# Performance work log

Measured on AMD Instinct MI355X. Metric: run time of the kernel, lower is better.

The kernel has to match this reference:

```python
import jax, jax.numpy as jnp
import numpy as np
from jax import lax

B, CIN, COUT, K, SDIM, H = 8, 512, 512, 3, 512, 32
EPS = 1e-8
LRELU_SLOPE = 0.2
ACT_SCALE = float(np.sqrt(2.0))


def setup_inputs() -> dict:
    key = jax.random.key(0)
    k1, k2, k3, k4 = jax.random.split(key, 4)
    return {
        "x": jax.random.normal(k1, (B, CIN, H, H), jnp.float32),
        "style": jax.random.normal(k2, (B, SDIM), jnp.float32),
        "weight": jax.random.normal(k3, (COUT, CIN, K, K), jnp.float32),
        "mod_w": jax.random.normal(k4, (CIN, SDIM), jnp.float32),
        "mod_b": jnp.ones((CIN,), jnp.float32),  # EqualLinear bias_init=1
        "bias": jnp.zeros((COUT,), jnp.float32),  # FusedLeakyReLU bias
    }


def _blur_kernel(c):
    bk = np.array([1.0, 3.0, 3.0, 1.0], np.float32)
    bk = bk[None, :] * bk[:, None]
    bk = bk / bk.sum() * 4.0  # upsample_factor ** 2
    return jnp.tile(jnp.asarray(bk)[None, None], (c, 1, 1, 1))  # (C,1,4,4)


def reference(x, style, weight, mod_w, mod_b, bias):
    b, cin, h, w = x.shape
    cout, k = weight.shape[0], weight.shape[-1]
    conv_scale = 1.0 / np.sqrt(cin * k * k)
    lin_scale = 1.0 / np.sqrt(mod_w.shape[1])

    # style modulation: EqualLinear(style_dim -> in_channel), bias_init=1
    s = style @ (mod_w * lin_scale).T + mod_b  # (B, Cin)

    # per-sample modulated weights (B, Cout, Cin, k, k)
    wmod = conv_scale * weight[None] * s[:, None, :, None, None]
    demod = lax.rsqrt(jnp.sum(wmod * wmod, axis=(2, 3, 4)) + EPS)
    wmod = wmod * demod[:, :, None, None, None]

    # conv_transpose2d(stride=2, pad=0) == conv with lhs_dilation=2, pad=k-1,
    # spatially-flipped kernel (torch transposes (Cout,Cin)->(Cin,Cout)).
    wflip = jnp.flip(wmod, (-2, -1))

    def convt(xi, wi):  # xi: (Cin,H,W), wi: (Cout,Cin,k,k)
        return lax.conv_general_dilated(
            xi[None], wi, (1, 1), [(k - 1, k - 1)] * 2,
            lhs_dilation=(2, 2),
            dimension_numbers=("NCHW", "OIHW", "NCHW"))[0]

    y = jax.vmap(convt)(x, wflip)  # (B, Cout, 2H+1, 2W+1)

    # Blur: upfirdn2d with pad=(1,1), depthwise 4x4 FIR (kernel symmetric)
    bk = _blur_kernel(cout)
    y = lax.conv_general_dilated(
        y, bk, (1, 1), [(1, 1), (1, 1)],
        feature_group_count=cout,
        dimension_numbers=("NCHW", "OIHW", "NCHW"))  # (B, Cout, 2H, 2W)

    # FusedLeakyReLU: leaky_relu(y + bias) * sqrt(2)
    z = y + bias[None, :, None, None]
    return jnp.where(z >= 0, z, LRELU_SLOPE * z) * ACT_SCALE
```

## Files before the change

kernel.cpp:

```cpp
#include <hip/hip_runtime.h>
#include <hip/hip_bf16.h>

#define NB 8
#define CIN 512
#define COUT 512
#define SDIM 512

typedef __attribute__((ext_vector_type(8))) short short8;
typedef __attribute__((ext_vector_type(4))) float f32x4;

static constexpr float CONV_SCALE = 0.014731391274719740f;
static constexpr float LIN_SCALE  = 0.044194173824159216f;

static constexpr size_t OFF_S     = 0;
static constexpr size_t OFF_WSQ   = 16384;
static constexpr size_t OFF_DEMOD = 1064960;
static constexpr size_t OFF_XP    = 1081344;
static constexpr size_t OFF_WP    = 10551296;
static constexpr size_t OFF_Y1    = 15269888;
static constexpr size_t XP_BYTES  = 9469952;

__device__ __forceinline__ int wpoff(int ps) {
  return ps == 0 ? 0 : ps == 1 ? 1048576 : ps == 2 ? 1572864 : 2097152;
}
__device__ __forceinline__ constexpr int y1off(int ps) {
  return ps == 0 ? 0 : ps == 1 ? 4460544 : ps == 2 ? 8785920 : 13111296;
}

__device__ __forceinline__ short f2bf(float f) {
  unsigned u = __builtin_bit_cast(unsigned, f);
  unsigned r = (u + 0x7fffu + ((u >> 16) & 1u)) >> 16;
  return (short)r;
}

__device__ __forceinline__ void load_lds16(const short* g, short* l) {
  __builtin_amdgcn_global_load_lds(
      (const __attribute__((address_space(1))) unsigned int*)g,
      (__attribute__((address_space(3))) unsigned int*)l, 16, 0, 0);
}

__global__ void k_style(const float* __restrict__ style, const float* __restrict__ mod_w,
                        const float* __restrict__ mod_b, float* __restrict__ s_out) {
  int wid = threadIdx.x >> 6, lane = threadIdx.x & 63;
  int ci = blockIdx.x * 4 + wid;
  float acc[NB] = {};
  for (int k = lane; k < SDIM; k += 64) {
    float wm = mod_w[ci * SDIM + k];
#pragma unroll
    for (int b = 0; b < NB; ++b) acc[b] += wm * style[b * SDIM + k];
  }
#pragma unroll
  for (int b = 0; b < NB; ++b) {
    float v = acc[b];
    for (int o = 32; o > 0; o >>= 1) v += __shfl_xor(v, o);
    if (lane == 0) s_out[b * CIN + ci] = v * LIN_SCALE + mod_b[ci];
  }
}

__global__ void k_wprep(const float* __restrict__ w, short* __restrict__ wp,
                        float* __restrict__ wsq) {
  int idx = blockIdx.x * blockDim.x + threadIdx.x;
  int co = idx >> 9, ci = idx & 511;
  float wv[3][3];
  float sq = 0.f;
#pragma unroll
  for (int i = 0; i < 9; ++i) {
    float v = w[idx * 9 + i];
    wv[i / 3][i % 3] = v;
    sq += v * v;
  }
  wsq[idx] = sq * CONV_SCALE * CONV_SCALE;
#pragma unroll
  for (int wy = 0; wy < 3; ++wy)
#pragma unroll
    for (int wx = 0; wx < 3; ++wx) {
      int psy = (wy == 1) ? 1 : 0, psx = (wx == 1) ? 1 : 0;
      int u = psy ? 0 : (wy == 0 ? 1 : 0);
      int v = psx ? 0 : (wx == 0 ? 1 : 0);
      int ps = psy * 2 + psx;
      int tap = psy ? (psx ? 0 : v) : (psx ? u : u * 2 + v);
      int k = tap * 512 + ci;
      int elem = wpoff(ps) + ((k >> 6) * 512 + co) * 64 + (k & 63);
      wp[elem] = f2bf(wv[wy][wx] * CONV_SCALE);
    }
}

__global__ void k_demod(const float* __restrict__ wsq, const float* __restrict__ s,
                        float* __restrict__ demod) {
  int wid = threadIdx.x >> 6, lane = threadIdx.x & 63;
  int co = blockIdx.x * 4 + wid;
  float acc[NB] = {};
  for (int ci = lane; ci < CIN; ci += 64) {
    float wq = wsq[co * CIN + ci];
#pragma unroll
    for (int b = 0; b < NB; ++b) {
      float sv = s[b * CIN + ci];
      acc[b] += wq * sv * sv;
    }
  }
#pragma unroll
  for (int b = 0; b < NB; ++b) {
    float v = acc[b];
    for (int o = 32; o > 0; o >>= 1) v += __shfl_xor(v, o);
    if (lane == 0) demod[b * COUT + co] = rsqrtf(v + 1e-8f);
  }
}

__global__ void k_xprep(const float* __restrict__ x, const float* __restrict__ s,
                        short* __restrict__ xp) {
  __shared__ float t[64][65];
  int sp0 = blockIdx.x * 64, ci0 = blockIdx.y * 64, b = blockIdx.z;
  for (int r = threadIdx.y; r < 64; r += 4)
    t[r][threadIdx.x] = x[(b * CIN + ci0 + r) * 1024 + sp0 + threadIdx.x];
  __syncthreads();
  int ci = ci0 + threadIdx.x;
  float sv = s[b * CIN + ci];
  for (int r = threadIdx.y; r < 64; r += 4) {
    int sp = sp0 + r;
    int yy = sp >> 5, xx = sp & 31;
    xp[((b * 34 + yy + 1) * 34 + (xx + 1)) * 512 + ci] = f2bf(t[threadIdx.x][r] * sv);
  }
}

__global__ __launch_bounds__(256, 2) void k_gemm(const short* __restrict__ xp,
                                                 const short* __restrict__ wp,
                                                 float* __restrict__ y1) {
  int ps = blockIdx.z;
  int psy = ps >> 1, psx = ps & 1;
  int Ny = 33 - psy, Nx = 33 - psx;
  int N = NB * Ny * Nx;
  int n0 = blockIdx.x * 128;
  if (n0 >= N) return;
  int m0 = blockIdx.y * 128;
  int KT = (2 - psy) * (2 - psx) * 8;
  const short* wpb = wp + wpoff(ps);
  float* y1b = y1 + y1off(ps);

  __shared__ short sW[128 * 64];
  __shared__ short sX[128 * 64];

  int tid = threadIdx.x;
  int wid = tid >> 6, lane = tid & 63;

  int bb[4], ay[4], ax[4];
#pragma unroll
  for (int i = 0; i < 4; ++i) {
    int seg = i * 256 + tid;
    int n = n0 + (seg >> 3);
    if (n >= N) n = N - 1;
    int b = n / (Ny * Nx);
    int rem = n - b * (Ny * Nx);
    int a_y = rem / Nx;
    bb[i] = b; ay[i] = a_y; ax[i] = rem - a_y * Nx;
  }
  int kseg8 = (tid & 7) * 8;

  f32x4 acc[4][4] = {};

  for (int kt = 0; kt < KT; ++kt) {
    int tap = kt >> 3, ci0 = (kt & 7) << 6;
    int oy, ox;
    if (ps == 0)      { oy = tap >> 1; ox = tap & 1; }
    else if (ps == 1) { oy = tap;      ox = 1; }
    else if (ps == 2) { oy = 1;        ox = tap; }
    else              { oy = 1;        ox = 1; }
#pragma unroll
    for (int i = 0; i < 4; ++i) {
      int seg = i * 256 + tid;
      const short* g = wpb + (kt * 512 + m0 + (seg >> 3)) * 64 + kseg8;
      load_lds16(g, &sW[(i * 4 + wid) * 512]);
    }
#pragma unroll
    for (int i = 0; i < 4; ++i) {
      const short* g = xp + ((bb[i] * 34 + ay[i] + oy) * 34 + ax[i] + ox) * 512 + ci0 + kseg8;
      load_lds16(g, &sX[(i * 4 + wid) * 512]);
    }
    asm volatile("s_waitcnt vmcnt(0)" ::: "memory");
    __syncthreads();

    int wm = (wid >> 1) * 64, wn = (wid & 1) * 64;
#pragma unroll
    for (int ks = 0; ks < 2; ++ks) {
      short8 af[4], bf[4];
#pragma unroll
      for (int mf = 0; mf < 4; ++mf)
        af[mf] = *(const short8*)&sW[(wm + mf * 16 + (lane & 15)) * 64 + ks * 32 + (lane >> 4) * 8];
#pragma unroll
      for (int nf = 0; nf < 4; ++nf)
        bf[nf] = *(const short8*)&sX[(wn + nf * 16 + (lane & 15)) * 64 + ks * 32 + (lane >> 4) * 8];
#pragma unroll
      for (int mf = 0; mf < 4; ++mf)
#pragma unroll
        for (int nf = 0; nf < 4; ++nf)
          acc[mf][nf] = __builtin_amdgcn_mfma_f32_16x16x32_bf16(af[mf], bf[nf], acc[mf][nf], 0, 0, 0);
    }
    __syncthreads();
  }

  int wm = (wid >> 1) * 64, wn = (wid & 1) * 64;
#pragma unroll
  for (int mf = 0; mf < 4; ++mf) {
    int m = m0 + wm + mf * 16 + (lane >> 4) * 4;
#pragma unroll
    for (int nf = 0; nf < 4; ++nf) {
      int n = n0 + wn + nf * 16 + (lane & 15);
      if (n < N) {
#pragma unroll
        for (int r = 0; r < 4; ++r) y1b[(m + r) * N + n] = acc[mf][nf][r];
      }
    }
  }
}

__global__ __launch_bounds__(256, 4) void k_blur(const float* __restrict__ y1,
                                                 const float* __restrict__ demod,
                                                 const float* __restrict__ bias,
                                                 float* __restrict__ out) {
  __shared__ float sin_[4][35 * 35];
  __shared__ float stmp[2][35][64];
  const int tid = threadIdx.x;
  const int bc = blockIdx.x;
  const int co = bc & 511, b = bc >> 9;

  for (int i = tid; i < 4 * 35 * 35; i += 256) ((float*)sin_)[i] = 0.f;
  __syncthreads();

#pragma unroll
  for (int ps = 0; ps < 4; ++ps) {
    const int Nyv = 33 - (ps >> 1), Nxv = 33 - (ps & 1);
    const float* pl = y1 + y1off(ps) + (co * NB + b) * (Nyv * Nxv);
    for (int t = tid; t < Nyv * Nxv; t += 256) {
      int av = t / Nxv, ah = t - av * Nxv;
      sin_[ps][(av + 1) * 35 + ah + 1] = pl[t];
    }
  }
  __syncthreads();

  const int q = tid & 63;
  const int mx = q >> 1, fx = q & 1;
  int xp0, xi0, xp1, xi1, xp2, xi2, xp3, xi3;
  if (fx) { xp0 = 0; xi0 = mx + 1; xp1 = 1; xi1 = mx + 1; xp2 = 0; xi2 = mx + 2; xp3 = 1; xi3 = mx + 2; }
  else    { xp0 = 1; xi0 = mx;     xp1 = 0; xi1 = mx + 1; xp2 = 1; xi2 = mx + 1; xp3 = 0; xi3 = mx + 2; }

  for (int r = tid >> 6; r < 70; r += 4) {
    int pv = (r >= 35) ? 1 : 0;
    int av = r - pv * 35;
    float v = 0.25f * sin_[pv * 2 + xp0][av * 35 + xi0]
            + 0.75f * sin_[pv * 2 + xp1][av * 35 + xi1]
            + 0.75f * sin_[pv * 2 + xp2][av * 35 + xi2]
            + 0.25f * sin_[pv * 2 + xp3][av * 35 + xi3];
    stmp[pv][av][q] = v;
  }
  __syncthreads();

  const float dm = demod[b * COUT + co], bs = bias[co];
  for (int p = tid >> 6; p < 64; p += 4) {
    int my = p >> 1, fy = p & 1;
    float v;
    if (fy) v = 0.25f * stmp[0][my + 1][q] + 0.75f * stmp[1][my + 1][q]
              + 0.75f * stmp[0][my + 2][q] + 0.25f * stmp[1][my + 2][q];
    else    v = 0.25f * stmp[1][my][q]     + 0.75f * stmp[0][my + 1][q]
              + 0.75f * stmp[1][my + 1][q] + 0.25f * stmp[0][my + 2][q];
    float val = dm * v + bs;
    out[(bc * 64 + p) * 64 + q] = (val >= 0.f ? val : 0.2f * val) * 1.41421356237309515f;
  }
}

extern "C" void kernel_launch(void* const* d_in, const int* in_sizes, int n_in,
                              void* d_out, int out_size, void* d_ws, size_t ws_size,
                              hipStream_t stream) {
  const float* x      = (const float*)d_in[0];
  const float* style  = (const float*)d_in[1];
  const float* weight = (const float*)d_in[2];
  const float* mod_w  = (const float*)d_in[3];
  const float* mod_b  = (const float*)d_in[4];
  const float* bias   = (const float*)d_in[5];
  float* out = (float*)d_out;
  char* ws = (char*)d_ws;

  float* s     = (float*)(ws + OFF_S);
  float* wsq   = (float*)(ws + OFF_WSQ);
  float* demod = (float*)(ws + OFF_DEMOD);
  short* xp    = (short*)(ws + OFF_XP);
  short* wp    = (short*)(ws + OFF_WP);
  float* y1    = (float*)(ws + OFF_Y1);

  hipMemsetAsync(xp, 0, XP_BYTES, stream);
  k_style<<<128, 256, 0, stream>>>(style, mod_w, mod_b, s);
  k_wprep<<<1024, 256, 0, stream>>>(weight, wp, wsq);
  k_demod<<<128, 256, 0, stream>>>(wsq, s, demod);
  k_xprep<<<dim3(16, 8, 8), dim3(64, 4), 0, stream>>>(x, s, xp);
  k_gemm<<<dim3(69, 4, 4), 256, 0, stream>>>(xp, wp, y1);
  k_blur<<<4096, 256, 0, stream>>>(y1, demod, bias, out);
}
```

Measured before the change: 142.6 us.

## Make GEMM persistent with atomic ticket work queue across parity phases

```diff
diff --git a/kernel.cpp b/kernel.cpp
--- a/kernel.cpp
+++ b/kernel.cpp
@@ -19,6 +19,9 @@
 static constexpr size_t OFF_WP    = 10551296;
 static constexpr size_t OFF_Y1    = 15269888;
 static constexpr size_t XP_BYTES  = 9469952;
+static constexpr size_t OFF_TICKET = OFF_WSQ;
+
+static constexpr int NJOBS = 1060;
 
 __device__ __forceinline__ int wpoff(int ps) {
   return ps == 0 ? 0 : ps == 1 ? 1048576 : ps == 2 ? 1572864 : 2097152;
@@ -124,89 +127,102 @@
 
 __global__ __launch_bounds__(256, 2) void k_gemm(const short* __restrict__ xp,
                                                  const short* __restrict__ wp,
-                                                 float* __restrict__ y1) {
-  int ps = blockIdx.z;
-  int psy = ps >> 1, psx = ps & 1;
-  int Ny = 33 - psy, Nx = 33 - psx;
-  int N = NB * Ny * Nx;
-  int n0 = blockIdx.x * 128;
-  if (n0 >= N) return;
-  int m0 = blockIdx.y * 128;
-  int KT = (2 - psy) * (2 - psx) * 8;
-  const short* wpb = wp + wpoff(ps);
-  float* y1b = y1 + y1off(ps);
-
+                                                 float* __restrict__ y1,
+                                                 unsigned int* __restrict__ ticket) {
   __shared__ short sW[128 * 64];
   __shared__ short sX[128 * 64];
-
-  int tid = threadIdx.x;
-  int wid = tid >> 6, lane = tid & 63;
-
-  int bb[4], ay[4], ax[4];
-#pragma unroll
-  for (int i = 0; i < 4; ++i) {
-    int seg = i * 256 + tid;
-    int n = n0 + (seg >> 3);
-    if (n >= N) n = N - 1;
-    int b = n / (Ny * Nx);
-    int rem = n - b * (Ny * Nx);
-    int a_y = rem / Nx;
-    bb[i] = b; ay[i] = a_y; ax[i] = rem - a_y * Nx;
-  }
-  int kseg8 = (tid & 7) * 8;
-
-  f32x4 acc[4][4] = {};
-
-  for (int kt = 0; kt < KT; ++kt) {
-    int tap = kt >> 3, ci0 = (kt & 7) << 6;
-    int oy, ox;
-    if (ps == 0)      { oy = tap >> 1; ox = tap & 1; }
-    else if (ps == 1) { oy = tap;      ox = 1; }
-    else if (ps == 2) { oy = 1;        ox = tap; }
-    else              { oy = 1;        ox = 1; }
+  __shared__ int sjob;
+
+  const int tid = threadIdx.x;
+  const int wid = tid >> 6, lane = tid & 63;
+  const int kseg8 = (tid & 7) * 8;
+  const int wm = (wid >> 1) * 64, wn = (wid & 1) * 64;
+
+  for (;;) {
+    __syncthreads();
+    if (tid == 0) sjob = (int)atomicAdd(ticket, 1u);
+    __syncthreads();
+    const int j = sjob;
+    if (j >= NJOBS) break;
+
+    int ps, base;
+    if (j < 276)      { ps = 0; base = 0; }
+    else if (j < 540) { ps = 1; base = 276; }
+    else if (j < 804) { ps = 2; base = 540; }
+    else              { ps = 3; base = 804; }
+    const int r = j - base;
+    const int nb = r >> 2, mb = r & 3;
+    const int psy = ps >> 1, psx = ps & 1;
+    const int Ny = 33 - psy, Nx = 33 - psx;
+    const int N = NB * Ny * Nx;
+    const int n0 = nb * 128, m0 = mb * 128;
+    const int KT = (2 - psy) * (2 - psx) * 8;
+    const short* wpb = wp + wpoff(ps);
+    float* y1b = y1 + y1off(ps);
+
+    int bb[4], ay[4], ax[4];
 #pragma unroll
     for (int i = 0; i < 4; ++i) {
       int seg = i * 256 + tid;
-      const short* g = wpb + (kt * 512 + m0 + (seg >> 3)) * 64 + kseg8;
-      load_lds16(g, &sW[(i * 4 + wid) * 512]);
-    }
-#pragma unroll
-    for (int i = 0; i < 4; ++i) {
-      const short* g = xp + ((bb[i] * 34 + ay[i] + oy) * 34 + ax[i] + ox) * 512 + ci0 + kseg8;
-      load_lds16(g, &sX[(i * 4 + wid) * 512]);
-    }
-    asm volatile("s_waitcnt vmcnt(0)" ::: "memory");
-    __syncthreads();
-
-    int wm = (wid >> 1) * 64, wn = (wid & 1) * 64;
-#pragma unroll
-    for (int ks = 0; ks < 2; ++ks) {
-      short8 af[4], bf[4];
-#pragma unroll
-      for (int mf = 0; mf < 4; ++mf)
-        af[mf] = *(const short8*)&sW[(wm + mf * 16 + (lane & 15)) * 64 + ks * 32 + (lane >> 4) * 8];
-#pragma unroll
-      for (int nf = 0; nf < 4; ++nf)
-        bf[nf] = *(const short8*)&sX[(wn + nf * 16 + (lane & 15)) * 64 + ks * 32 + (lane >> 4) * 8];
-#pragma unroll
-      for (int mf = 0; mf < 4; ++mf)
+      int n = n0 + (seg >> 3);
+      if (n >= N) n = N - 1;
+      int b = n / (Ny * Nx);
+      int rem = n - b * (Ny * Nx);
+      int a_y = rem / Nx;
+      bb[i] = b; ay[i] = a_y; ax[i] = rem - a_y * Nx;
+    }
+
+    f32x4 acc[4][4] = {};
+
+    for (int kt = 0; kt < KT; ++kt) {
+      int tap = kt >> 3, ci0 = (kt & 7) << 6;
+      int oy, ox;
+      if (ps == 0)      { oy = tap >> 1; ox = tap & 1; }
+      else if (ps == 1) { oy = tap;      ox = 1; }
+      else if (ps == 2) { oy = 1;        ox = tap; }
+      else              { oy = 1;        ox = 1; }
+#pragma unroll
+      for (int i = 0; i < 4; ++i) {
+        int seg = i * 256 + tid;
+        const short* g = wpb + (kt * 512 + m0 + (seg >> 3)) * 64 + kseg8;
+        load_lds16(g, &sW[(i * 4 + wid) * 512]);
+      }
+#pragma unroll
+      for (int i = 0; i < 4; ++i) {
+        const short* g = xp + ((bb[i] * 34 + ay[i] + oy) * 34 + ax[i] + ox) * 512 + ci0 + kseg8;
+        load_lds16(g, &sX[(i * 4 + wid) * 512]);
+      }
+      asm volatile("s_waitcnt vmcnt(0)" ::: "memory");
+      __syncthreads();
+
+#pragma unroll
+      for (int ks = 0; ks < 2; ++ks) {
+        short8 af[4], bf[4];
+#pragma unroll
+        for (int mf = 0; mf < 4; ++mf)
+          af[mf] = *(const short8*)&sW[(wm + mf * 16 + (lane & 15)) * 64 + ks * 32 + (lane >> 4) * 8];
 #pragma unroll
         for (int nf = 0; nf < 4; ++nf)
-          acc[mf][nf] = __builtin_amdgcn_mfma_f32_16x16x32_bf16(af[mf], bf[nf], acc[mf][nf], 0, 0, 0);
-    }
-    __syncthreads();
-  }
-
-  int wm = (wid >> 1) * 64, wn = (wid & 1) * 64;
-#pragma unroll
-  for (int mf = 0; mf < 4; ++mf) {
-    int m = m0 + wm + mf * 16 + (lane >> 4) * 4;
-#pragma unroll
-    for (int nf = 0; nf < 4; ++nf) {
-      int n = n0 + wn + nf * 16 + (lane & 15);
-      if (n < N) {
-#pragma unroll
-        for (int r = 0; r < 4; ++r) y1b[(m + r) * N + n] = acc[mf][nf][r];
+          bf[nf] = *(const short8*)&sX[(wn + nf * 16 + (lane & 15)) * 64 + ks * 32 + (lane >> 4) * 8];
+#pragma unroll
+        for (int mf = 0; mf < 4; ++mf)
+#pragma unroll
+          for (int nf = 0; nf < 4; ++nf)
+            acc[mf][nf] = __builtin_amdgcn_mfma_f32_16x16x32_bf16(af[mf], bf[nf], acc[mf][nf], 0, 0, 0);
+      }
+      __syncthreads();
+    }
+
+#pragma unroll
+    for (int mf = 0; mf < 4; ++mf) {
+      int m = m0 + wm + mf * 16 + (lane >> 4) * 4;
+#pragma unroll
+      for (int nf = 0; nf < 4; ++nf) {
+        int n = n0 + wn + nf * 16 + (lane & 15);
+        if (n < N) {
+#pragma unroll
+          for (int rr = 0; rr < 4; ++rr) y1b[(m + rr) * N + n] = acc[mf][nf][rr];
+        }
       }
     }
   }
@@ -281,6 +297,7 @@
   float* s     = (float*)(ws + OFF_S);
   float* wsq   = (float*)(ws + OFF_WSQ);
   float* demod = (float*)(ws + OFF_DEMOD);
+  unsigned int* ticket = (unsigned int*)(ws + OFF_TICKET);
   short* xp    = (short*)(ws + OFF_XP);
   short* wp    = (short*)(ws + OFF_WP);
   float* y1    = (float*)(ws + OFF_Y1);
@@ -289,7 +306,8 @@
   k_style<<<128, 256, 0, stream>>>(style, mod_w, mod_b, s);
   k_wprep<<<1024, 256, 0, stream>>>(weight, wp, wsq);
   k_demod<<<128, 256, 0, stream>>>(wsq, s, demod);
+  hipMemsetAsync(ticket, 0, 4, stream);
   k_xprep<<<dim3(16, 8, 8), dim3(64, 4), 0, stream>>>(x, s, xp);
-  k_gemm<<<dim3(69, 4, 4), 256, 0, stream>>>(xp, wp, y1);
+  k_gemm<<<1024, 256, 0, stream>>>(xp, wp, y1, ticket);
   k_blur<<<4096, 256, 0, stream>>>(y1, demod, bias, out);
 }
```

Result: slower. 153.4 us (+7.6%).
